# Optimization experiments

Measured on AMD Instinct MI355X. Metric: run time of the kernel, lower is better.

Reference implementation:

```python
import jax, jax.numpy as jnp
import numpy as np

N_EMB = 1024
HEAD_SIZE = 64
BLOCK_SIZE = 2048
B, T = 8, 2048


def setup_inputs() -> dict:
    key = jax.random.key(0)
    kx, kq, kk, kv = jax.random.split(key, 4)
    scale = 1.0 / (N_EMB ** 0.5)
    x = jax.random.normal(kx, (B, T, N_EMB), dtype=jnp.float32)
    Wq = jax.random.uniform(kq, (N_EMB, HEAD_SIZE), dtype=jnp.float32) * scale
    Wk = jax.random.uniform(kk, (N_EMB, HEAD_SIZE), dtype=jnp.float32) * scale
    Wv = jax.random.uniform(kv, (N_EMB, HEAD_SIZE), dtype=jnp.float32) * scale
    return {"x": x, "Wq": Wq, "Wk": Wk, "Wv": Wv}


def reference(x, Wq, Wk, Wv):
    # Faithful to Head.__call__ with is_training=False.
    # NOTE: original code applies NO 1/sqrt(head_size) scaling to the scores.
    Bt, Tt, _ = x.shape
    q = x @ Wq                      # (B, T, H)
    k = x @ Wk                      # (B, T, H)
    v = x @ Wv                      # (B, T, H)
    wei = jnp.einsum('bth,bsh->bts', q, k)  # (B, T, T)
    causal = jnp.tril(jnp.ones((Tt, Tt), dtype=bool))
    wei = jnp.where(causal, wei, -jnp.inf)
    wei = jax.nn.softmax(wei, axis=-1)
    out = jnp.einsum('bts,bsh->bth', wei, v)  # (B, T, H)
    return out
```

## Files before the change

kernel.cpp:

```cpp
#include <hip/hip_runtime.h>
#include <hip/hip_bf16.h>

#define BB 8
#define TT 2048
#define EE 1024
#define HH 64

typedef __attribute__((ext_vector_type(8))) short short8;
typedef __attribute__((ext_vector_type(4))) float f32x4;

__device__ inline f32x4 mfma_16x16x32(short8 a, short8 b, f32x4 c) {
  return __builtin_amdgcn_mfma_f32_16x16x32_bf16(a, b, c, 0, 0, 0);
}

__device__ inline void gload_lds16(const __hip_bfloat16* g, __hip_bfloat16* l) {
  __builtin_amdgcn_global_load_lds((const __attribute__((address_space(1))) void*)g,
                                   (__attribute__((address_space(3))) void*)l,
                                   16, 0, 0);
}

__device__ inline short f2bf(float f) {
  __hip_bfloat16 h = __float2bfloat16(f);
  return *reinterpret_cast<short*>(&h);
}
__device__ inline float bf2f(short s) {
  __hip_bfloat16 h = *reinterpret_cast<__hip_bfloat16*>(&s);
  return __bfloat162float(h);
}

#define WAIT_LGKM0() __builtin_amdgcn_s_waitcnt(0xC07F)

__global__ void prep_w(const float* __restrict__ Wq, const float* __restrict__ Wk,
                       const float* __restrict__ Wv,
                       __hip_bfloat16* __restrict__ Wthi,
                       __hip_bfloat16* __restrict__ Wtlo) {
  const int n = blockIdx.x;
  const int m = n >> 6;
  const int h = n & 63;
  const float* W = (m == 0) ? Wq : (m == 1) ? Wk : Wv;
  const int e0 = threadIdx.x * 4;
#pragma unroll
  for (int j = 0; j < 4; ++j) {
    const float w = W[(e0 + j) * 64 + h];
    const __hip_bfloat16 hi = __float2bfloat16(w);
    Wthi[n * 1024 + e0 + j] = hi;
    Wtlo[n * 1024 + e0 + j] = __float2bfloat16(w - __bfloat162float(hi));
  }
}

__global__ __launch_bounds__(256) void qkv_gemm(
    const float* __restrict__ x,
    const __hip_bfloat16* __restrict__ Wthi, const __hip_bfloat16* __restrict__ Wtlo,
    __hip_bfloat16* __restrict__ qhi, __hip_bfloat16* __restrict__ qlo,
    __hip_bfloat16* __restrict__ khi, __hip_bfloat16* __restrict__ klo,
    __hip_bfloat16* __restrict__ vT) {
  __shared__ __hip_bfloat16 Ahi[2][32 * 72];
  __shared__ __hip_bfloat16 Alo[2][32 * 72];
  __shared__ __hip_bfloat16 Bhi[2][192 * 64];

  const int tid  = threadIdx.x;
  const int wave = tid >> 6;
  const int lane = tid & 63;
  const int row0 = blockIdx.x * 32;
  const int l15 = lane & 15, l4 = lane >> 4;

  const int lr = tid >> 3;
  const int le = (tid & 7) * 8;
  const float* xrow = x + (row0 + lr) * 1024 + le;

  f32x4 acc[2][3];
#pragma unroll
  for (int m = 0; m < 2; ++m)
#pragma unroll
    for (int j = 0; j < 3; ++j) acc[m][j] = f32x4{0.f, 0.f, 0.f, 0.f};

  auto issue_Bhi = [&](int c, int buf) {
    const int g = (lane & 7) ^ ((lane >> 3) & 7);
#pragma unroll
    for (int s = 0; s < 3; ++s) {
      const int j = wave + s * 4;
#pragma unroll
      for (int qh = 0; qh < 2; ++qh) {
        const int qq = j * 2 + qh;
        const int n  = qq * 8 + (lane >> 3);
        gload_lds16(Wthi + n * 1024 + c * 64 + g * 8, &Bhi[buf][qq * 512]);
      }
    }
  };
  auto load_Blo = [&](int c, short8* bl) {
#pragma unroll
    for (int jj = 0; jj < 2; ++jj) {
      const int j = wave + jj * 4;
      const __hip_bfloat16* p = Wtlo + (j * 16 + l15) * 1024 + c * 64;
      bl[jj * 2]     = *(const short8*)(p + l4 * 8);
      bl[jj * 2 + 1] = *(const short8*)(p + 32 + l4 * 8);
    }
  };
  auto write_A = [&](int buf, const f32x4* xr) {
    short8 h0, l0;
    const float* xf = (const float*)xr;
#pragma unroll
    for (int j = 0; j < 8; ++j) {
      const float v = xf[j];
      const short h = f2bf(v);
      h0[j] = h;
      l0[j] = f2bf(v - bf2f(h));
    }
    *(short8*)&Ahi[buf][lr * 72 + le] = h0;
    *(short8*)&Alo[buf][lr * 72 + le] = l0;
  };
  auto compute = [&](int buf, const short8* bl) {
#pragma unroll
    for (int m = 0; m < 2; ++m) {
      const int tr = m * 16 + l15;
      short8 ah0 = *(const short8*)&Ahi[buf][tr * 72 + l4 * 8];
      short8 ah1 = *(const short8*)&Ahi[buf][tr * 72 + 32 + l4 * 8];
      short8 al0 = *(const short8*)&Alo[buf][tr * 72 + l4 * 8];
      short8 al1 = *(const short8*)&Alo[buf][tr * 72 + 32 + l4 * 8];
#pragma unroll
      for (int jj = 0; jj < 3; ++jj) {
        const int j  = (jj < 2) ? (wave + jj * 4) : (wave + 8);
        const int n  = j * 16 + l15;
        const int o0 = ((l4)     ^ (n & 7)) * 8;
        const int o1 = ((4 + l4) ^ (n & 7)) * 8;
        short8 bh0 = *(const short8*)&Bhi[buf][n * 64 + o0];
        short8 bh1 = *(const short8*)&Bhi[buf][n * 64 + o1];
        acc[m][jj] = mfma_16x16x32(ah0, bh0, acc[m][jj]);
        acc[m][jj] = mfma_16x16x32(ah1, bh1, acc[m][jj]);
        if (jj < 2) {
          acc[m][jj] = mfma_16x16x32(ah0, bl[jj * 2],     acc[m][jj]);
          acc[m][jj] = mfma_16x16x32(ah1, bl[jj * 2 + 1], acc[m][jj]);
          acc[m][jj] = mfma_16x16x32(al0, bh0, acc[m][jj]);
          acc[m][jj] = mfma_16x16x32(al1, bh1, acc[m][jj]);
        }
      }
    }
  };

  f32x4 xr[2], xn[2];
  {
    const f32x4* p = (const f32x4*)xrow;
    xr[0] = p[0]; xr[1] = p[1];
  }
  short8 blc[4], bln[4];
  issue_Bhi(0, 0);
  load_Blo(0, blc);
  __builtin_amdgcn_s_waitcnt(0);
  write_A(0, xr);
  __syncthreads();

  for (int c = 0; c < 16; ++c) {
    const int p = c & 1;
    if (c < 15) {
      const f32x4* pp = (const f32x4*)(xrow + (c + 1) * 64);
      xn[0] = pp[0]; xn[1] = pp[1];
      issue_Bhi(c + 1, p ^ 1);
      load_Blo(c + 1, bln);
    }
    compute(p, blc);
    if (c < 15) {
      __builtin_amdgcn_s_waitcnt(0);
      write_A(p ^ 1, xn);
#pragma unroll
      for (int q = 0; q < 4; ++q) blc[q] = bln[q];
    }
    __syncthreads();
  }

  const int hcol = wave * 16 + l15;
#pragma unroll
  for (int jj = 0; jj < 3; ++jj) {
#pragma unroll
    for (int m = 0; m < 2; ++m) {
#pragma unroll
      for (int r = 0; r < 4; ++r) {
        const int trow = row0 + m * 16 + l4 * 4 + r;
        const float val = acc[m][jj][r];
        if (jj == 0) {
          const __hip_bfloat16 hi = __float2bfloat16(val);
          qhi[trow * 64 + hcol] = hi;
          qlo[trow * 64 + hcol] = __float2bfloat16(val - __bfloat162float(hi));
        } else if (jj == 1) {
          const __hip_bfloat16 hi = __float2bfloat16(val);
          khi[trow * 64 + hcol] = hi;
          klo[trow * 64 + hcol] = __float2bfloat16(val - __bfloat162float(hi));
        } else {
          const int bb = trow >> 11, tl = trow & 2047;
          vT[(bb * 64 + hcol) * 2048 + tl] = __float2bfloat16(val);
        }
      }
    }
  }
}

__global__ __launch_bounds__(256, 4) void attn(
    const __hip_bfloat16* __restrict__ qhi, const __hip_bfloat16* __restrict__ qlo,
    const __hip_bfloat16* __restrict__ khi, const __hip_bfloat16* __restrict__ klo,
    const __hip_bfloat16* __restrict__ vT, float* __restrict__ out) {
  __shared__ __hip_bfloat16 Psm[4][16 * 72];
  __shared__ float Osm[4][16][65];
  __shared__ float Msm[4][16];
  __shared__ float Lsm[4][16];

  const int tid  = threadIdx.x;
  const int wave = tid >> 6;
  const int lane = tid & 63;
  const int l15 = lane & 15, l4 = lane >> 4;

  const int b  = blockIdx.x & 7;
  const int ss = 127 - (blockIdx.x >> 3);
  const int t0 = ss * 16;
  const int ntiles = (ss >> 2) + 1;

  const __hip_bfloat16* qph = qhi + (b * 2048 + t0 + l15) * 64;
  const __hip_bfloat16* qpl = qlo + (b * 2048 + t0 + l15) * 64;
  const short8 qh0 = *(const short8*)(qph + l4 * 8);
  const short8 qh1 = *(const short8*)(qph + 32 + l4 * 8);
  const short8 ql0 = *(const short8*)(qpl + l4 * 8);
  const short8 ql1 = *(const short8*)(qpl + 32 + l4 * 8);

  f32x4 acc[4];
#pragma unroll
  for (int j = 0; j < 4; ++j) acc[j] = f32x4{0.f, 0.f, 0.f, 0.f};
  float m_[4], l_[4];
#pragma unroll
  for (int r = 0; r < 4; ++r) { m_[r] = -1e30f; l_[r] = 0.f; }

  const __hip_bfloat16* kbase_h = khi + (size_t)b * 2048 * 64;
  const __hip_bfloat16* kbase_l = klo + (size_t)b * 2048 * 64;
  const __hip_bfloat16* vbase   = vT + (size_t)b * 64 * 2048;

  for (int kt = wave; kt < ntiles; kt += 4) {
    const int k0 = kt << 6;
    const bool diag = (kt == ntiles - 1);

    f32x4 s_[4];
#pragma unroll
    for (int j = 0; j < 4; ++j) {
      if (diag && (k0 + j * 16) > (t0 + 15)) {
        s_[j] = f32x4{-1e30f, -1e30f, -1e30f, -1e30f};
      } else {
        const __hip_bfloat16* kph = kbase_h + (k0 + j * 16 + l15) * 64;
        const __hip_bfloat16* kpl = kbase_l + (k0 + j * 16 + l15) * 64;
        const short8 kh0 = *(const short8*)(kph + l4 * 8);
        const short8 kh1 = *(const short8*)(kph + 32 + l4 * 8);
        const short8 kl0 = *(const short8*)(kpl + l4 * 8);
        const short8 kl1 = *(const short8*)(kpl + 32 + l4 * 8);
        f32x4 z = f32x4{0.f, 0.f, 0.f, 0.f};
        z = mfma_16x16x32(qh0, kh0, z);
        z = mfma_16x16x32(qh1, kh1, z);
        z = mfma_16x16x32(qh0, kl0, z);
        z = mfma_16x16x32(qh1, kl1, z);
        z = mfma_16x16x32(ql0, kh0, z);
        z = mfma_16x16x32(ql1, kh1, z);
        s_[j] = z;
      }
    }
    if (diag) {
#pragma unroll
      for (int j = 0; j < 4; ++j) {
        const int key = k0 + j * 16 + l15;
#pragma unroll
        for (int r = 0; r < 4; ++r) {
          const int row = t0 + l4 * 4 + r;
          if (key > row) s_[j][r] = -1e30f;
        }
      }
    }

    float mx[4], rs[4], al[4];
#pragma unroll
    for (int r = 0; r < 4; ++r)
      mx[r] = fmaxf(fmaxf(s_[0][r], s_[1][r]), fmaxf(s_[2][r], s_[3][r]));
    for (int off = 1; off < 16; off <<= 1) {
#pragma unroll
      for (int r = 0; r < 4; ++r) mx[r] = fmaxf(mx[r], __shfl_xor(mx[r], off));
    }
#pragma unroll
    for (int r = 0; r < 4; ++r) {
      const float mn = fmaxf(m_[r], mx[r]);
      al[r] = __expf(m_[r] - mn);
      m_[r] = mn;
      rs[r] = 0.f;
    }
#pragma unroll
    for (int j = 0; j < 4; ++j) {
#pragma unroll
      for (int r = 0; r < 4; ++r) {
        const float pv = __expf(s_[j][r] - m_[r]);
        s_[j][r] = pv;
        rs[r] += pv;
      }
    }
    for (int off = 1; off < 16; off <<= 1) {
#pragma unroll
      for (int r = 0; r < 4; ++r) rs[r] += __shfl_xor(rs[r], off);
    }
#pragma unroll
    for (int r = 0; r < 4; ++r) l_[r] = l_[r] * al[r] + rs[r];
#pragma unroll
    for (int j = 0; j < 4; ++j)
#pragma unroll
      for (int r = 0; r < 4; ++r) acc[j][r] *= al[r];

#pragma unroll
    for (int j = 0; j < 4; ++j)
#pragma unroll
      for (int r = 0; r < 4; ++r)
        Psm[wave][(l4 * 4 + r) * 72 + j * 16 + l15] = __float2bfloat16(s_[j][r]);

    short8 vf0[4], vf1[4];
#pragma unroll
    for (int j = 0; j < 4; ++j) {
      const __hip_bfloat16* vp = vbase + (j * 16 + l15) * 2048 + k0;
      vf0[j] = *(const short8*)(vp + l4 * 8);
      vf1[j] = *(const short8*)(vp + 32 + l4 * 8);
    }

    WAIT_LGKM0();

    const short8 pf0 = *(const short8*)&Psm[wave][l15 * 72 + l4 * 8];
    const short8 pf1 = *(const short8*)&Psm[wave][l15 * 72 + 32 + l4 * 8];
#pragma unroll
    for (int j = 0; j < 4; ++j) {
      acc[j] = mfma_16x16x32(pf0, vf0[j], acc[j]);
      acc[j] = mfma_16x16x32(pf1, vf1[j], acc[j]);
    }
  }

#pragma unroll
  for (int j = 0; j < 4; ++j)
#pragma unroll
    for (int r = 0; r < 4; ++r)
      Osm[wave][l4 * 4 + r][j * 16 + l15] = acc[j][r];
  if (l15 == 0) {
#pragma unroll
    for (int r = 0; r < 4; ++r) {
      Msm[wave][l4 * 4 + r] = m_[r];
      Lsm[wave][l4 * 4 + r] = l_[r];
    }
  }
  __syncthreads();

#pragma unroll
  for (int rr = 0; rr < 4; ++rr) {
    const int row = wave * 4 + rr;
    float M = fmaxf(fmaxf(Msm[0][row], Msm[1][row]),
                    fmaxf(Msm[2][row], Msm[3][row]));
    float L = 0.f, O = 0.f;
#pragma unroll
    for (int w2 = 0; w2 < 4; ++w2) {
      const float a = __expf(Msm[w2][row] - M);
      L += a * Lsm[w2][row];
      O += a * Osm[w2][row][lane];
    }
    out[(b * 2048 + t0 + row) * 64 + lane] = O / L;
  }
}

extern "C" void kernel_launch(void* const* d_in, const int* in_sizes, int n_in,
                              void* d_out, int out_size, void* d_ws, size_t ws_size,
                              hipStream_t stream) {
  const float* x  = (const float*)d_in[0];
  const float* Wq = (const float*)d_in[1];
  const float* Wk = (const float*)d_in[2];
  const float* Wv = (const float*)d_in[3];
  float* out = (float*)d_out;

  char* ws = (char*)d_ws;
  __hip_bfloat16* Wthi = (__hip_bfloat16*)ws;
  __hip_bfloat16* Wtlo = (__hip_bfloat16*)(ws + 393216);
  __hip_bfloat16* qhi  = (__hip_bfloat16*)(ws + 786432);
  __hip_bfloat16* qlo  = (__hip_bfloat16*)(ws + 786432 + 1 * 2097152);
  __hip_bfloat16* khi  = (__hip_bfloat16*)(ws + 786432 + 2 * 2097152);
  __hip_bfloat16* klo  = (__hip_bfloat16*)(ws + 786432 + 3 * 2097152);
  __hip_bfloat16* vT   = (__hip_bfloat16*)(ws + 786432 + 4 * 2097152);

  prep_w<<<192, 256, 0, stream>>>(Wq, Wk, Wv, Wthi, Wtlo);
  qkv_gemm<<<512, 256, 0, stream>>>(x, Wthi, Wtlo, qhi, qlo, khi, klo, vT);
  attn<<<1024, 256, 0, stream>>>(qhi, qlo, khi, klo, vT, out);
}
```

Baseline: 183.0 us.

## Pair long and short causal query tiles per block and hoist K/V loads

Each attention block now handles two 16-row query tiles, one from the end and one from the start of the sequence, so every block does about the same amount of causal work. The grid is halved to 512 blocks. K and V fragment loads are also issued together before the QK MFMAs and softmax, giving memory latency more time to overlap with compute. In exchange, each block runs longer and needs an extra barrier between the two halves. Holding more K/V registers at once may also raise register pressure and cut occupancy.

```diff
diff --git a/kernel.cpp b/kernel.cpp
--- a/kernel.cpp
+++ b/kernel.cpp
@@ -208,153 +208,166 @@
   const int l15 = lane & 15, l4 = lane >> 4;
 
   const int b  = blockIdx.x & 7;
-  const int ss = 127 - (blockIdx.x >> 3);
-  const int t0 = ss * 16;
-  const int ntiles = (ss >> 2) + 1;
-
-  const __hip_bfloat16* qph = qhi + (b * 2048 + t0 + l15) * 64;
-  const __hip_bfloat16* qpl = qlo + (b * 2048 + t0 + l15) * 64;
-  const short8 qh0 = *(const short8*)(qph + l4 * 8);
-  const short8 qh1 = *(const short8*)(qph + 32 + l4 * 8);
-  const short8 ql0 = *(const short8*)(qpl + l4 * 8);
-  const short8 ql1 = *(const short8*)(qpl + 32 + l4 * 8);
-
-  f32x4 acc[4];
-#pragma unroll
-  for (int j = 0; j < 4; ++j) acc[j] = f32x4{0.f, 0.f, 0.f, 0.f};
-  float m_[4], l_[4];
-#pragma unroll
-  for (int r = 0; r < 4; ++r) { m_[r] = -1e30f; l_[r] = 0.f; }
+  const int pp = blockIdx.x >> 3;
 
   const __hip_bfloat16* kbase_h = khi + (size_t)b * 2048 * 64;
   const __hip_bfloat16* kbase_l = klo + (size_t)b * 2048 * 64;
   const __hip_bfloat16* vbase   = vT + (size_t)b * 64 * 2048;
 
-  for (int kt = wave; kt < ntiles; kt += 4) {
-    const int k0 = kt << 6;
-    const bool diag = (kt == ntiles - 1);
-
-    f32x4 s_[4];
-#pragma unroll
-    for (int j = 0; j < 4; ++j) {
-      if (diag && (k0 + j * 16) > (t0 + 15)) {
-        s_[j] = f32x4{-1e30f, -1e30f, -1e30f, -1e30f};
-      } else {
-        const __hip_bfloat16* kph = kbase_h + (k0 + j * 16 + l15) * 64;
-        const __hip_bfloat16* kpl = kbase_l + (k0 + j * 16 + l15) * 64;
-        const short8 kh0 = *(const short8*)(kph + l4 * 8);
-        const short8 kh1 = *(const short8*)(kph + 32 + l4 * 8);
-        const short8 kl0 = *(const short8*)(kpl + l4 * 8);
-        const short8 kl1 = *(const short8*)(kpl + 32 + l4 * 8);
-        f32x4 z = f32x4{0.f, 0.f, 0.f, 0.f};
-        z = mfma_16x16x32(qh0, kh0, z);
-        z = mfma_16x16x32(qh1, kh1, z);
-        z = mfma_16x16x32(qh0, kl0, z);
-        z = mfma_16x16x32(qh1, kl1, z);
-        z = mfma_16x16x32(ql0, kh0, z);
-        z = mfma_16x16x32(ql1, kh1, z);
-        s_[j] = z;
-      }
-    }
-    if (diag) {
-#pragma unroll
-      for (int j = 0; j < 4; ++j) {
-        const int key = k0 + j * 16 + l15;
+  for (int half = 0; half < 2; ++half) {
+    const int ss = half ? pp : (127 - pp);
+    const int t0 = ss * 16;
+    const int ntiles = (ss >> 2) + 1;
+
+    const __hip_bfloat16* qph = qhi + (b * 2048 + t0 + l15) * 64;
+    const __hip_bfloat16* qpl = qlo + (b * 2048 + t0 + l15) * 64;
+    const short8 qh0 = *(const short8*)(qph + l4 * 8);
+    const short8 qh1 = *(const short8*)(qph + 32 + l4 * 8);
+    const short8 ql0 = *(const short8*)(qpl + l4 * 8);
+    const short8 ql1 = *(const short8*)(qpl + 32 + l4 * 8);
+
+    f32x4 acc[4];
+#pragma unroll
+    for (int j = 0; j < 4; ++j) acc[j] = f32x4{0.f, 0.f, 0.f, 0.f};
+    float m_[4], l_[4];
+#pragma unroll
+    for (int r = 0; r < 4; ++r) { m_[r] = -1e30f; l_[r] = 0.f; }
+
+    for (int kt = wave; kt < ntiles; kt += 4) {
+      const int k0 = kt << 6;
+      const bool diag = (kt == ntiles - 1);
+
+      short8 kh0[4], kh1[4], kl0[4], kl1[4];
+#pragma unroll
+      for (int j = 0; j < 4; ++j) {
+        if (!(diag && (k0 + j * 16) > (t0 + 15))) {
+          const __hip_bfloat16* kph = kbase_h + (k0 + j * 16 + l15) * 64;
+          const __hip_bfloat16* kpl = kbase_l + (k0 + j * 16 + l15) * 64;
+          kh0[j] = *(const short8*)(kph + l4 * 8);
+          kh1[j] = *(const short8*)(kph + 32 + l4 * 8);
+          kl0[j] = *(const short8*)(kpl + l4 * 8);
+          kl1[j] = *(const short8*)(kpl + 32 + l4 * 8);
+        }
+      }
+
+      f32x4 s_[4];
+#pragma unroll
+      for (int j = 0; j < 4; ++j) {
+        if (diag && (k0 + j * 16) > (t0 + 15)) {
+          s_[j] = f32x4{-1e30f, -1e30f, -1e30f, -1e30f};
+        } else {
+          f32x4 z = f32x4{0.f, 0.f, 0.f, 0.f};
+          z = mfma_16x16x32(qh0, kh0[j], z);
+          z = mfma_16x16x32(qh1, kh1[j], z);
+          z = mfma_16x16x32(qh0, kl0[j], z);
+          z = mfma_16x16x32(qh1, kl1[j], z);
+          z = mfma_16x16x32(ql0, kh0[j], z);
+          z = mfma_16x16x32(ql1, kh1[j], z);
+          s_[j] = z;
+        }
+      }
+
+      short8 vf0[4], vf1[4];
+#pragma unroll
+      for (int j = 0; j < 4; ++j) {
+        const __hip_bfloat16* vp = vbase + (j * 16 + l15) * 2048 + k0;
+        vf0[j] = *(const short8*)(vp + l4 * 8);
+        vf1[j] = *(const short8*)(vp + 32 + l4 * 8);
+      }
+
+      if (diag) {
+#pragma unroll
+        for (int j = 0; j < 4; ++j) {
+          const int key = k0 + j * 16 + l15;
+#pragma unroll
+          for (int r = 0; r < 4; ++r) {
+            const int row = t0 + l4 * 4 + r;
+            if (key > row) s_[j][r] = -1e30f;
+          }
+        }
+      }
+
+      float mx[4], rs[4], al[4];
+#pragma unroll
+      for (int r = 0; r < 4; ++r)
+        mx[r] = fmaxf(fmaxf(s_[0][r], s_[1][r]), fmaxf(s_[2][r], s_[3][r]));
+      for (int off = 1; off < 16; off <<= 1) {
+#pragma unroll
+        for (int r = 0; r < 4; ++r) mx[r] = fmaxf(mx[r], __shfl_xor(mx[r], off));
+      }
+#pragma unroll
+      for (int r = 0; r < 4; ++r) {
+        const float mn = fmaxf(m_[r], mx[r]);
+        al[r] = __expf(m_[r] - mn);
+        m_[r] = mn;
+        rs[r] = 0.f;
+      }
+#pragma unroll
+      for (int j = 0; j < 4; ++j) {
 #pragma unroll
         for (int r = 0; r < 4; ++r) {
-          const int row = t0 + l4 * 4 + r;
-          if (key > row) s_[j][r] = -1e30f;
-        }
-      }
-    }
-
-    float mx[4], rs[4], al[4];
-#pragma unroll
-    for (int r = 0; r < 4; ++r)
-      mx[r] = fmaxf(fmaxf(s_[0][r], s_[1][r]), fmaxf(s_[2][r], s_[3][r]));
-    for (int off = 1; off < 16; off <<= 1) {
-#pragma unroll
-      for (int r = 0; r < 4; ++r) mx[r] = fmaxf(mx[r], __shfl_xor(mx[r], off));
-    }
-#pragma unroll
-    for (int r = 0; r < 4; ++r) {
-      const float mn = fmaxf(m_[r], mx[r]);
-      al[r] = __expf(m_[r] - mn);
-      m_[r] = mn;
-      rs[r] = 0.f;
-    }
-#pragma unroll
-    for (int j = 0; j < 4; ++j) {
+          const float pv = __expf(s_[j][r] - m_[r]);
+          s_[j][r] = pv;
+          rs[r] += pv;
+        }
+      }
+      for (int off = 1; off < 16; off <<= 1) {
+#pragma unroll
+        for (int r = 0; r < 4; ++r) rs[r] += __shfl_xor(rs[r], off);
+      }
+#pragma unroll
+      for (int r = 0; r < 4; ++r) l_[r] = l_[r] * al[r] + rs[r];
+#pragma unroll
+      for (int j = 0; j < 4; ++j)
+#pragma unroll
+        for (int r = 0; r < 4; ++r) acc[j][r] *= al[r];
+
+#pragma unroll
+      for (int j = 0; j < 4; ++j)
+#pragma unroll
+        for (int r = 0; r < 4; ++r)
+          Psm[wave][(l4 * 4 + r) * 72 + j * 16 + l15] = __float2bfloat16(s_[j][r]);
+
+      WAIT_LGKM0();
+
+      const short8 pf0 = *(const short8*)&Psm[wave][l15 * 72 + l4 * 8];
+      const short8 pf1 = *(const short8*)&Psm[wave][l15 * 72 + 32 + l4 * 8];
+#pragma unroll
+      for (int j = 0; j < 4; ++j) {
+        acc[j] = mfma_16x16x32(pf0, vf0[j], acc[j]);
+        acc[j] = mfma_16x16x32(pf1, vf1[j], acc[j]);
+      }
+    }
+
+#pragma unroll
+    for (int j = 0; j < 4; ++j)
+#pragma unroll
+      for (int r = 0; r < 4; ++r)
+        Osm[wave][l4 * 4 + r][j * 16 + l15] = acc[j][r];
+    if (l15 == 0) {
 #pragma unroll
       for (int r = 0; r < 4; ++r) {
-        const float pv = __expf(s_[j][r] - m_[r]);
-        s_[j][r] = pv;
-        rs[r] += pv;
-      }
-    }
-    for (int off = 1; off < 16; off <<= 1) {
-#pragma unroll
-      for (int r = 0; r < 4; ++r) rs[r] += __shfl_xor(rs[r], off);
-    }
-#pragma unroll
-    for (int r = 0; r < 4; ++r) l_[r] = l_[r] * al[r] + rs[r];
-#pragma unroll
-    for (int j = 0; j < 4; ++j)
-#pragma unroll
-      for (int r = 0; r < 4; ++r) acc[j][r] *= al[r];
-
-#pragma unroll
-    for (int j = 0; j < 4; ++j)
-#pragma unroll
-      for (int r = 0; r < 4; ++r)
-        Psm[wave][(l4 * 4 + r) * 72 + j * 16 + l15] = __float2bfloat16(s_[j][r]);
-
-    short8 vf0[4], vf1[4];
-#pragma unroll
-    for (int j = 0; j < 4; ++j) {
-      const __hip_bfloat16* vp = vbase + (j * 16 + l15) * 2048 + k0;
-      vf0[j] = *(const short8*)(vp + l4 * 8);
-      vf1[j] = *(const short8*)(vp + 32 + l4 * 8);
-    }
-
-    WAIT_LGKM0();
-
-    const short8 pf0 = *(const short8*)&Psm[wave][l15 * 72 + l4 * 8];
-    const short8 pf1 = *(const short8*)&Psm[wave][l15 * 72 + 32 + l4 * 8];
-#pragma unroll
-    for (int j = 0; j < 4; ++j) {
-      acc[j] = mfma_16x16x32(pf0, vf0[j], acc[j]);
-      acc[j] = mfma_16x16x32(pf1, vf1[j], acc[j]);
-    }
-  }
-
-#pragma unroll
-  for (int j = 0; j < 4; ++j)
-#pragma unroll
-    for (int r = 0; r < 4; ++r)
-      Osm[wave][l4 * 4 + r][j * 16 + l15] = acc[j][r];
-  if (l15 == 0) {
-#pragma unroll
-    for (int r = 0; r < 4; ++r) {
-      Msm[wave][l4 * 4 + r] = m_[r];
-      Lsm[wave][l4 * 4 + r] = l_[r];
-    }
-  }
-  __syncthreads();
-
-#pragma unroll
-  for (int rr = 0; rr < 4; ++rr) {
-    const int row = wave * 4 + rr;
-    float M = fmaxf(fmaxf(Msm[0][row], Msm[1][row]),
-                    fmaxf(Msm[2][row], Msm[3][row]));
-    float L = 0.f, O = 0.f;
-#pragma unroll
-    for (int w2 = 0; w2 < 4; ++w2) {
-      const float a = __expf(Msm[w2][row] - M);
-      L += a * Lsm[w2][row];
-      O += a * Osm[w2][row][lane];
-    }
-    out[(b * 2048 + t0 + row) * 64 + lane] = O / L;
+        Msm[wave][l4 * 4 + r] = m_[r];
+        Lsm[wave][l4 * 4 + r] = l_[r];
+      }
+    }
+    __syncthreads();
+
+#pragma unroll
+    for (int rr = 0; rr < 4; ++rr) {
+      const int row = wave * 4 + rr;
+      float M = fmaxf(fmaxf(Msm[0][row], Msm[1][row]),
+                      fmaxf(Msm[2][row], Msm[3][row]));
+      float L = 0.f, O = 0.f;
+#pragma unroll
+      for (int w2 = 0; w2 < 4; ++w2) {
+        const float a = __expf(Msm[w2][row] - M);
+        L += a * Lsm[w2][row];
+        O += a * Osm[w2][row][lane];
+      }
+      out[(b * 2048 + t0 + row) * 64 + lane] = O / L;
+    }
+    __syncthreads();
   }
 }
 
@@ -378,5 +391,5 @@
 
   prep_w<<<192, 256, 0, stream>>>(Wq, Wk, Wv, Wthi, Wtlo);
   qkv_gemm<<<512, 256, 0, stream>>>(x, Wthi, Wtlo, qhi, qlo, khi, klo, vT);
-  attn<<<1024, 256, 0, stream>>>(qhi, qlo, khi, klo, vT, out);
-}
+  attn<<<512, 256, 0, stream>>>(qhi, qlo, khi, klo, vT, out);
+}
```

Measured after the change: 245.4 us. +34.2%, slower.

## Replace online softmax max tracking with a Cauchy-Schwarz score bound

Applied to the files above, without the earlier changes.

Adds a small kernel that computes the per-batch maximum squared key norm with atomics. The attention kernel then uses |q|*max|k|+2 as a fixed per-row softmax offset instead of the running max. This removes the per-tile max and sum shuffles, the rescale of the accumulators, and the cross-wave max merge; the row sum is now produced by an extra MFMA against a vector of ones. It also batches key loads in pairs and relaxes the launch-bounds occupancy hint, at the cost of an extra launch and a risk of exp underflow when the bound far exceeds the true scores.

```diff
diff --git a/kernel.cpp b/kernel.cpp
--- a/kernel.cpp
+++ b/kernel.cpp
@@ -33,8 +33,10 @@
 __global__ void prep_w(const float* __restrict__ Wq, const float* __restrict__ Wk,
                        const float* __restrict__ Wv,
                        __hip_bfloat16* __restrict__ Wthi,
-                       __hip_bfloat16* __restrict__ Wtlo) {
+                       __hip_bfloat16* __restrict__ Wtlo,
+                       float* __restrict__ maxk2) {
   const int n = blockIdx.x;
+  if (n == 0 && threadIdx.x < 8) maxk2[threadIdx.x] = 0.f;
   const int m = n >> 6;
   const int h = n & 63;
   const float* W = (m == 0) ? Wq : (m == 1) ? Wk : Wv;
@@ -193,13 +195,36 @@
   }
 }
 
-__global__ __launch_bounds__(256, 4) void attn(
+__global__ __launch_bounds__(256) void knorm(
+    const __hip_bfloat16* __restrict__ khi, const __hip_bfloat16* __restrict__ klo,
+    float* __restrict__ maxk2) {
+  const int row = blockIdx.x * 256 + threadIdx.x;
+  const int b = row >> 11;
+  const __hip_bfloat16* ph = khi + row * 64;
+  const __hip_bfloat16* pl = klo + row * 64;
+  float s = 0.f;
+#pragma unroll
+  for (int i = 0; i < 8; ++i) {
+    const short8 h = *(const short8*)(ph + i * 8);
+    const short8 l = *(const short8*)(pl + i * 8);
+#pragma unroll
+    for (int j = 0; j < 8; ++j) {
+      const float v = bf2f(h[j]) + bf2f(l[j]);
+      s += v * v;
+    }
+  }
+  for (int off = 1; off < 64; off <<= 1) s = fmaxf(s, __shfl_xor(s, off));
+  if ((threadIdx.x & 63) == 0)
+    atomicMax((int*)&maxk2[b], __float_as_int(s));
+}
+
+__global__ __launch_bounds__(256, 2) void attn(
     const __hip_bfloat16* __restrict__ qhi, const __hip_bfloat16* __restrict__ qlo,
     const __hip_bfloat16* __restrict__ khi, const __hip_bfloat16* __restrict__ klo,
-    const __hip_bfloat16* __restrict__ vT, float* __restrict__ out) {
+    const __hip_bfloat16* __restrict__ vT, const float* __restrict__ maxk2,
+    float* __restrict__ out) {
   __shared__ __hip_bfloat16 Psm[4][16 * 72];
   __shared__ float Osm[4][16][65];
-  __shared__ float Msm[4][16];
   __shared__ float Lsm[4][16];
 
   const int tid  = threadIdx.x;
@@ -219,12 +244,29 @@
   const short8 ql0 = *(const short8*)(qpl + l4 * 8);
   const short8 ql1 = *(const short8*)(qpl + 32 + l4 * 8);
 
+  float qn = 0.f;
+#pragma unroll
+  for (int i = 0; i < 8; ++i) {
+    const float v0 = bf2f(qh0[i]) + bf2f(ql0[i]);
+    const float v1 = bf2f(qh1[i]) + bf2f(ql1[i]);
+    qn += v0 * v0 + v1 * v1;
+  }
+  qn += __shfl_xor(qn, 16);
+  qn += __shfl_xor(qn, 32);
+  const float kmax = sqrtf(maxk2[b]);
+  const float crow = sqrtf(qn) * kmax + 2.0f;
+  float c_[4];
+#pragma unroll
+  for (int r = 0; r < 4; ++r) c_[r] = __shfl(crow, l4 * 4 + r);
+
+  short8 ones;
+#pragma unroll
+  for (int i = 0; i < 8; ++i) ones[i] = (short)0x3F80;
+
   f32x4 acc[4];
 #pragma unroll
   for (int j = 0; j < 4; ++j) acc[j] = f32x4{0.f, 0.f, 0.f, 0.f};
-  float m_[4], l_[4];
-#pragma unroll
-  for (int r = 0; r < 4; ++r) { m_[r] = -1e30f; l_[r] = 0.f; }
+  f32x4 accL = f32x4{0.f, 0.f, 0.f, 0.f};
 
   const __hip_bfloat16* kbase_h = khi + (size_t)b * 2048 * 64;
   const __hip_bfloat16* kbase_l = klo + (size_t)b * 2048 * 64;
@@ -236,26 +278,38 @@
 
     f32x4 s_[4];
 #pragma unroll
-    for (int j = 0; j < 4; ++j) {
-      if (diag && (k0 + j * 16) > (t0 + 15)) {
-        s_[j] = f32x4{-1e30f, -1e30f, -1e30f, -1e30f};
-      } else {
-        const __hip_bfloat16* kph = kbase_h + (k0 + j * 16 + l15) * 64;
-        const __hip_bfloat16* kpl = kbase_l + (k0 + j * 16 + l15) * 64;
-        const short8 kh0 = *(const short8*)(kph + l4 * 8);
-        const short8 kh1 = *(const short8*)(kph + 32 + l4 * 8);
-        const short8 kl0 = *(const short8*)(kpl + l4 * 8);
-        const short8 kl1 = *(const short8*)(kpl + 32 + l4 * 8);
-        f32x4 z = f32x4{0.f, 0.f, 0.f, 0.f};
-        z = mfma_16x16x32(qh0, kh0, z);
-        z = mfma_16x16x32(qh1, kh1, z);
-        z = mfma_16x16x32(qh0, kl0, z);
-        z = mfma_16x16x32(qh1, kl1, z);
-        z = mfma_16x16x32(ql0, kh0, z);
-        z = mfma_16x16x32(ql1, kh1, z);
-        s_[j] = z;
-      }
-    }
+    for (int st = 0; st < 2; ++st) {
+      short8 kh0[2], kh1[2], kl0[2], kl1[2];
+#pragma unroll
+      for (int jj = 0; jj < 2; ++jj) {
+        const int j = st * 2 + jj;
+        if (!(diag && (k0 + j * 16) > (t0 + 15))) {
+          const __hip_bfloat16* kph = kbase_h + (k0 + j * 16 + l15) * 64;
+          const __hip_bfloat16* kpl = kbase_l + (k0 + j * 16 + l15) * 64;
+          kh0[jj] = *(const short8*)(kph + l4 * 8);
+          kh1[jj] = *(const short8*)(kph + 32 + l4 * 8);
+          kl0[jj] = *(const short8*)(kpl + l4 * 8);
+          kl1[jj] = *(const short8*)(kpl + 32 + l4 * 8);
+        }
+      }
+#pragma unroll
+      for (int jj = 0; jj < 2; ++jj) {
+        const int j = st * 2 + jj;
+        if (diag && (k0 + j * 16) > (t0 + 15)) {
+          s_[j] = f32x4{-1e30f, -1e30f, -1e30f, -1e30f};
+        } else {
+          f32x4 z = f32x4{0.f, 0.f, 0.f, 0.f};
+          z = mfma_16x16x32(qh0, kh0[jj], z);
+          z = mfma_16x16x32(qh1, kh1[jj], z);
+          z = mfma_16x16x32(qh0, kl0[jj], z);
+          z = mfma_16x16x32(qh1, kl1[jj], z);
+          z = mfma_16x16x32(ql0, kh0[jj], z);
+          z = mfma_16x16x32(ql1, kh1[jj], z);
+          s_[j] = z;
+        }
+      }
+    }
+
     if (diag) {
 #pragma unroll
       for (int j = 0; j < 4; ++j) {
@@ -268,40 +322,10 @@
       }
     }
 
-    float mx[4], rs[4], al[4];
-#pragma unroll
-    for (int r = 0; r < 4; ++r)
-      mx[r] = fmaxf(fmaxf(s_[0][r], s_[1][r]), fmaxf(s_[2][r], s_[3][r]));
-    for (int off = 1; off < 16; off <<= 1) {
-#pragma unroll
-      for (int r = 0; r < 4; ++r) mx[r] = fmaxf(mx[r], __shfl_xor(mx[r], off));
-    }
-#pragma unroll
-    for (int r = 0; r < 4; ++r) {
-      const float mn = fmaxf(m_[r], mx[r]);
-      al[r] = __expf(m_[r] - mn);
-      m_[r] = mn;
-      rs[r] = 0.f;
-    }
-#pragma unroll
-    for (int j = 0; j < 4; ++j) {
-#pragma unroll
-      for (int r = 0; r < 4; ++r) {
-        const float pv = __expf(s_[j][r] - m_[r]);
-        s_[j][r] = pv;
-        rs[r] += pv;
-      }
-    }
-    for (int off = 1; off < 16; off <<= 1) {
-#pragma unroll
-      for (int r = 0; r < 4; ++r) rs[r] += __shfl_xor(rs[r], off);
-    }
-#pragma unroll
-    for (int r = 0; r < 4; ++r) l_[r] = l_[r] * al[r] + rs[r];
 #pragma unroll
     for (int j = 0; j < 4; ++j)
 #pragma unroll
-      for (int r = 0; r < 4; ++r) acc[j][r] *= al[r];
+      for (int r = 0; r < 4; ++r) s_[j][r] = __expf(s_[j][r] - c_[r]);
 
 #pragma unroll
     for (int j = 0; j < 4; ++j)
@@ -326,6 +350,8 @@
       acc[j] = mfma_16x16x32(pf0, vf0[j], acc[j]);
       acc[j] = mfma_16x16x32(pf1, vf1[j], acc[j]);
     }
+    accL = mfma_16x16x32(pf0, ones, accL);
+    accL = mfma_16x16x32(pf1, ones, accL);
   }
 
 #pragma unroll
@@ -335,25 +361,16 @@
       Osm[wave][l4 * 4 + r][j * 16 + l15] = acc[j][r];
   if (l15 == 0) {
 #pragma unroll
-    for (int r = 0; r < 4; ++r) {
-      Msm[wave][l4 * 4 + r] = m_[r];
-      Lsm[wave][l4 * 4 + r] = l_[r];
-    }
+    for (int r = 0; r < 4; ++r) Lsm[wave][l4 * 4 + r] = accL[r];
   }
   __syncthreads();
 
 #pragma unroll
   for (int rr = 0; rr < 4; ++rr) {
     const int row = wave * 4 + rr;
-    float M = fmaxf(fmaxf(Msm[0][row], Msm[1][row]),
-                    fmaxf(Msm[2][row], Msm[3][row]));
-    float L = 0.f, O = 0.f;
-#pragma unroll
-    for (int w2 = 0; w2 < 4; ++w2) {
-      const float a = __expf(Msm[w2][row] - M);
-      L += a * Lsm[w2][row];
-      O += a * Osm[w2][row][lane];
-    }
+    const float L = Lsm[0][row] + Lsm[1][row] + Lsm[2][row] + Lsm[3][row];
+    float O = Osm[0][row][lane] + Osm[1][row][lane] +
+              Osm[2][row][lane] + Osm[3][row][lane];
     out[(b * 2048 + t0 + row) * 64 + lane] = O / L;
   }
 }
@@ -375,8 +392,10 @@
   __hip_bfloat16* khi  = (__hip_bfloat16*)(ws + 786432 + 2 * 2097152);
   __hip_bfloat16* klo  = (__hip_bfloat16*)(ws + 786432 + 3 * 2097152);
   __hip_bfloat16* vT   = (__hip_bfloat16*)(ws + 786432 + 4 * 2097152);
-
-  prep_w<<<192, 256, 0, stream>>>(Wq, Wk, Wv, Wthi, Wtlo);
+  float* maxk2         = (float*)(ws + 786432 + 5 * 2097152);
+
+  prep_w<<<192, 256, 0, stream>>>(Wq, Wk, Wv, Wthi, Wtlo, maxk2);
   qkv_gemm<<<512, 256, 0, stream>>>(x, Wthi, Wtlo, qhi, qlo, khi, klo, vT);
-  attn<<<1024, 256, 0, stream>>>(qhi, qlo, khi, klo, vT, out);
-}
+  knorm<<<64, 256, 0, stream>>>(khi, klo, maxk2);
+  attn<<<1024, 256, 0, stream>>>(qhi, qlo, khi, klo, vT, maxk2, out);
+}
```

After: 184.9 us. About the same (+1.1%).
